# Kernel tuning notes

Hardware: AMD Instinct MI355X
Metric: run time of the kernel (lower is better)

## Reference

```python
import jax, jax.numpy as jnp
import numpy as np

# cost weights from __init__
W_CLASS = 1.0
W_KPTS = 1.0
W_CTRS = 1.0
W_DELTAS = 1.0
W_KPTS_CLASS = 1.0


def setup_inputs() -> dict:
    key = jax.random.key(0)
    k1, k2, k3, k4 = jax.random.split(key, 4)
    bs, Q, C, P = 16, 300, 2, 320
    pred_logits = jax.random.normal(k1, (bs, Q, C), dtype=jnp.float32)
    pred_kpts = jax.random.uniform(k2, (bs, Q, 53), dtype=jnp.float32)
    tgt_kpts = jax.random.uniform(k3, (P, 54), dtype=jnp.float32)
    # all visibility flags == 1 so the `if all(tgt_kpts[:,2])` branch is taken
    tgt_kpts = tgt_kpts.at[:, 2::3].set(1.0)
    tgt_ids = jax.random.randint(k4, (P,), 0, C)
    return {"pred_logits": pred_logits, "pred_kpts": pred_kpts,
            "tgt_kpts": tgt_kpts, "tgt_ids": tgt_ids}


def _cost_matrix(pred_logits, pred_kpts, tgt_kpts, tgt_ids):
    bs, Q, C = pred_logits.shape
    N = bs * Q
    P = tgt_kpts.shape[0]

    out_prob = jax.nn.softmax(pred_logits.reshape(N, C), axis=-1)  # [N,C]
    out_k = pred_kpts.reshape(N, -1)                               # [N,53]

    cost_class = -out_prob[:, tgt_ids]                             # [N,P]

    out_kpts_ids = out_k[:, 4::3]                                  # [N,17]
    tgt_kpts_ids = tgt_kpts[:, 5::3]                               # [P,17]

    x = jnp.concatenate([out_k[:, 0:1], out_k[:, 2::3]], axis=1)   # [N,18]
    y = jnp.concatenate([out_k[:, 1:2], out_k[:, 3::3]], axis=1)   # [N,18]
    x_abs = jnp.concatenate([x[:, 0:1], (x[:, 1:] - 0.5) * 2.0 + x[:, 0:1]], axis=1)
    y_abs = jnp.concatenate([y[:, 0:1], (y[:, 1:] - 0.5) * 2.0 + y[:, 0:1]], axis=1)

    tgt_x = tgt_kpts[:, 0::3]                                      # [P,18]
    tgt_y = tgt_kpts[:, 1::3]                                      # [P,18]
    tgt_x_abs = jnp.concatenate([tgt_x[:, 0:1], (tgt_x[:, 1:] - 0.5) * 2.0 + tgt_x[:, 0:1]], axis=1)
    tgt_y_abs = jnp.concatenate([tgt_y[:, 0:1], (tgt_y[:, 1:] - 0.5) * 2.0 + tgt_y[:, 0:1]], axis=1)

    vis = (tgt_kpts[:, 2::3] == 1.0).astype(pred_kpts.dtype)       # [P,18]
    visT = vis.T                                                   # [18,P]

    def interleave_pred(xc, yc):
        # [N,18,P] masked per target, interleaved to [N,36,P]
        mx = xc[:, :, None] * visT[None, :, :]
        my = yc[:, :, None] * visT[None, :, :]
        return jnp.stack([mx, my], axis=2).reshape(N, 36, P)

    def interleave_tgt(xc, yc):
        return jnp.stack([xc * vis, yc * vis], axis=2).reshape(P, 36)

    ok = interleave_pred(x, y)                 # [N,36,P]
    tk = interleave_tgt(tgt_x, tgt_y)          # [P,36]
    ok_abs = interleave_pred(x_abs, y_abs)     # [N,36,P]
    tk_abs = interleave_tgt(tgt_x_abs, tgt_y_abs)

    # vectorized version of the per-person cdist loop
    cost_deltas = jnp.abs(ok[:, 2:, :] - tk.T[None, 2:, :]).sum(axis=1)          # L1, [N,P]
    cost_kpts = jnp.abs(ok_abs[:, 2:, :] - tk_abs.T[None, 2:, :]).sum(axis=1)    # L1, [N,P]
    cost_ctrs = jnp.sqrt(((ok[:, :2, :] - tk.T[None, :2, :]) ** 2).sum(axis=1))  # L2, [N,P]
    cost_kpts_class = jnp.sqrt(((out_kpts_ids[:, None, :] - tgt_kpts_ids[None, :, :]) ** 2).sum(-1))  # [N,P]

    Cmat = (W_KPTS * cost_kpts + W_CTRS * cost_ctrs + W_DELTAS * cost_deltas
            + W_CLASS * cost_class + W_KPTS_CLASS * cost_kpts_class)
    return Cmat.reshape(bs, Q, P)


def reference(pred_logits, pred_kpts, tgt_kpts, tgt_ids):
    return _cost_matrix(pred_logits, pred_kpts, tgt_kpts, tgt_ids)
```

## Files before the change

kernel.cpp:

```cpp
#include <hip/hip_runtime.h>
#include <math.h>

#define BS 16
#define QN 300
#define CN 2
#define PN 320
#define NN (BS * QN)
#define KPRED 53
#define KTGT 54
#define TILE_N 4
#define STAGE_N (TILE_N * KPRED + TILE_N * CN)

__global__ __launch_bounds__(PN) void hungarian_cost_kernel(
    const float* __restrict__ pred_logits,
    const float* __restrict__ pred_kpts,
    const float* __restrict__ tgt_kpts,
    const int*   __restrict__ tgt_ids,
    float* __restrict__ out)
{
    __shared__ float sk[STAGE_N];
    const int p  = threadIdx.x;
    const int n0 = blockIdx.x * TILE_N;

    if (p < STAGE_N) {
        sk[p] = (p < TILE_N * KPRED)
                    ? pred_kpts[(size_t)n0 * KPRED + p]
                    : pred_logits[n0 * CN + (p - TILE_N * KPRED)];
    }

    float tx[18], ty[18], vjf[18], w[17];
    {
        const float* t = tgt_kpts + (size_t)p * KTGT;
        #pragma unroll
        for (int j = 0; j < 18; ++j) {
            tx[j] = t[3 * j];
            ty[j] = t[3 * j + 1];
            const float vv = t[3 * j + 2];
            vjf[j] = (vv == 1.0f) ? 1.0f : 0.0f;
            if (j >= 1) w[j - 1] = vv;
        }
    }
    const int cls = tgt_ids[p];

    __syncthreads();

    #pragma unroll
    for (int ni = 0; ni < TILE_N; ++ni) {
        const int n = n0 + ni;
        const float* k = &sk[ni * KPRED];

        const float dx0 = k[0] - tx[0];
        const float dy0 = k[1] - ty[0];

        float cd = 0.0f;
        float ck = 0.0f;
        float cq = 0.0f;
        #pragma unroll
        for (int j = 1; j < 18; ++j) {
            const float dx = k[3 * j - 1] - tx[j];
            const float dy = k[3 * j]     - ty[j];
            cd = fmaf(vjf[j], fabsf(dx) + fabsf(dy), cd);
            const float ax = fmaf(2.0f, dx, dx0);
            const float ay = fmaf(2.0f, dy, dy0);
            ck = fmaf(vjf[j], fabsf(ax) + fabsf(ay), ck);
            const float d = k[3 * j + 1] - w[j - 1];
            cq = fmaf(d, d, cq);
        }

        const float cc = vjf[0] * sqrtf(fmaf(dx0, dx0, dy0 * dy0));

        const float l0 = sk[TILE_N * KPRED + 2 * ni];
        const float l1 = sk[TILE_N * KPRED + 2 * ni + 1];
        const float m  = fmaxf(l0, l1);
        const float e0 = __expf(l0 - m);
        const float e1 = __expf(l1 - m);
        const float inv = 1.0f / (e0 + e1);
        const float ccls = -((cls == 0) ? e0 : e1) * inv;

        out[(size_t)n * PN + p] = ck + cc + cd + ccls + sqrtf(cq);
    }
}

extern "C" void kernel_launch(void* const* d_in, const int* in_sizes, int n_in,
                              void* d_out, int out_size, void* d_ws, size_t ws_size,
                              hipStream_t stream) {
    const float* pred_logits = (const float*)d_in[0];
    const float* pred_kpts   = (const float*)d_in[1];
    const float* tgt_kpts    = (const float*)d_in[2];
    const int*   tgt_ids     = (const int*)d_in[3];
    float* out = (float*)d_out;

    dim3 grid(NN / TILE_N);
    dim3 block(PN);
    hipLaunchKernelGGL(hungarian_cost_kernel, grid, block, 0, stream,
                       pred_logits, pred_kpts, tgt_kpts, tgt_ids, out);
}
```

Baseline: 75.06 us.

## Use persistent grid with double-buffered shared staging of prediction rows

Switches from one block per 4 prediction rows to a fixed grid of 960 blocks, each processing 5 rows strided by the grid size. The next row's keypoints and logits are prefetched into a second shared buffer while the current row is computed. The per-target registers are loaded once per block and reused across more rows, which cuts the redundant target loads the 1200-block launch performed. The cost is a block-wide barrier per row and fewer blocks in flight to hide memory latency.

```diff
diff --git a/kernel.cpp b/kernel.cpp
--- a/kernel.cpp
+++ b/kernel.cpp
@@ -8,8 +8,10 @@
 #define NN (BS * QN)
 #define KPRED 53
 #define KTGT 54
-#define TILE_N 4
-#define STAGE_N (TILE_N * KPRED + TILE_N * CN)
+
+#define GRID 960
+#define ROWS (NN / GRID)
+#define SROW 56
 
 __global__ __launch_bounds__(PN) void hungarian_cost_kernel(
     const float* __restrict__ pred_logits,
@@ -18,15 +20,9 @@
     const int*   __restrict__ tgt_ids,
     float* __restrict__ out)
 {
-    __shared__ float sk[STAGE_N];
-    const int p  = threadIdx.x;
-    const int n0 = blockIdx.x * TILE_N;
-
-    if (p < STAGE_N) {
-        sk[p] = (p < TILE_N * KPRED)
-                    ? pred_kpts[(size_t)n0 * KPRED + p]
-                    : pred_logits[n0 * CN + (p - TILE_N * KPRED)];
-    }
+    __shared__ float sk[2][SROW];
+    const int p   = threadIdx.x;
+    const int bid = blockIdx.x;
 
     float tx[18], ty[18], vjf[18], w[17];
     {
@@ -42,12 +38,22 @@
     }
     const int cls = tgt_ids[p];
 
+    if (p < KPRED)          sk[0][p] = pred_kpts[(size_t)bid * KPRED + p];
+    else if (p < KPRED + 2) sk[0][p] = pred_logits[(size_t)bid * CN + (p - KPRED)];
     __syncthreads();
 
     #pragma unroll
-    for (int ni = 0; ni < TILE_N; ++ni) {
-        const int n = n0 + ni;
-        const float* k = &sk[ni * KPRED];
+    for (int i = 0; i < ROWS; ++i) {
+        const int n   = bid + i * GRID;
+        const int cur = i & 1;
+
+        {
+            const int nn_ = (i + 1 < ROWS) ? (n + GRID) : n;
+            if (p < KPRED)          sk[cur ^ 1][p] = pred_kpts[(size_t)nn_ * KPRED + p];
+            else if (p < KPRED + 2) sk[cur ^ 1][p] = pred_logits[(size_t)nn_ * CN + (p - KPRED)];
+        }
+
+        const float* k = sk[cur];
 
         const float dx0 = k[0] - tx[0];
         const float dy0 = k[1] - ty[0];
@@ -69,15 +75,15 @@
 
         const float cc = vjf[0] * sqrtf(fmaf(dx0, dx0, dy0 * dy0));
 
-        const float l0 = sk[TILE_N * KPRED + 2 * ni];
-        const float l1 = sk[TILE_N * KPRED + 2 * ni + 1];
+        const float l0 = k[KPRED], l1 = k[KPRED + 1];
         const float m  = fmaxf(l0, l1);
         const float e0 = __expf(l0 - m);
         const float e1 = __expf(l1 - m);
-        const float inv = 1.0f / (e0 + e1);
-        const float ccls = -((cls == 0) ? e0 : e1) * inv;
+        const float ccls = -((cls == 0) ? e0 : e1) / (e0 + e1);
 
         out[(size_t)n * PN + p] = ck + cc + cd + ccls + sqrtf(cq);
+
+        __syncthreads();
     }
 }
 
@@ -90,8 +96,6 @@
     const int*   tgt_ids     = (const int*)d_in[3];
     float* out = (float*)d_out;
 
-    dim3 grid(NN / TILE_N);
-    dim3 block(PN);
-    hipLaunchKernelGGL(hungarian_cost_kernel, grid, block, 0, stream,
+    hipLaunchKernelGGL(hungarian_cost_kernel, dim3(GRID), dim3(PN), 0, stream,
                        pred_logits, pred_kpts, tgt_kpts, tgt_ids, out);
 }
```

Result: slower. 82.01 us (+9.3%).

## Drop LDS staging, read predictions directly and pack two rows into float2 math

Applied to the files above, without the earlier changes.

Removes the shared-memory staging of prediction keypoints and logits along with the block barrier. Each thread now reads the prediction values straight from global memory as uniform loads. The per-row arithmetic is paired across two query rows using 2-wide float vectors, so the compiler can emit packed FMA instructions. The cost is that every thread issues redundant global/scalar loads instead of LDS reads, and the gain depends on whether the compiler turns these into scalar loads and packed math.

```diff
diff --git a/kernel.cpp b/kernel.cpp
--- a/kernel.cpp
+++ b/kernel.cpp
@@ -9,7 +9,12 @@
 #define KPRED 53
 #define KTGT 54
 #define TILE_N 4
-#define STAGE_N (TILE_N * KPRED + TILE_N * CN)
+
+typedef float v2f __attribute__((ext_vector_type(2)));
+
+static __device__ __forceinline__ v2f fma2(v2f a, v2f b, v2f c) {
+    return __builtin_elementwise_fma(a, b, c);
+}
 
 __global__ __launch_bounds__(PN) void hungarian_cost_kernel(
     const float* __restrict__ pred_logits,
@@ -18,15 +23,8 @@
     const int*   __restrict__ tgt_ids,
     float* __restrict__ out)
 {
-    __shared__ float sk[STAGE_N];
     const int p  = threadIdx.x;
     const int n0 = blockIdx.x * TILE_N;
-
-    if (p < STAGE_N) {
-        sk[p] = (p < TILE_N * KPRED)
-                    ? pred_kpts[(size_t)n0 * KPRED + p]
-                    : pred_logits[n0 * CN + (p - TILE_N * KPRED)];
-    }
 
     float tx[18], ty[18], vjf[18], w[17];
     {
@@ -42,42 +40,64 @@
     }
     const int cls = tgt_ids[p];
 
-    __syncthreads();
+    #pragma unroll
+    for (int h = 0; h < TILE_N / 2; ++h) {
+        const int na = n0 + 2 * h;
+        const int nb = na + 1;
+        const float* ka = pred_kpts + (size_t)na * KPRED;
+        const float* kb = pred_kpts + (size_t)nb * KPRED;
 
-    #pragma unroll
-    for (int ni = 0; ni < TILE_N; ++ni) {
-        const int n = n0 + ni;
-        const float* k = &sk[ni * KPRED];
+        const v2f k0  = {ka[0], kb[0]};
+        const v2f k1  = {ka[1], kb[1]};
+        const v2f dx0 = k0 - (v2f){tx[0], tx[0]};
+        const v2f dy0 = k1 - (v2f){ty[0], ty[0]};
 
-        const float dx0 = k[0] - tx[0];
-        const float dy0 = k[1] - ty[0];
-
-        float cd = 0.0f;
-        float ck = 0.0f;
-        float cq = 0.0f;
+        v2f cd = {0.0f, 0.0f};
+        v2f ck = {0.0f, 0.0f};
+        v2f cq = {0.0f, 0.0f};
         #pragma unroll
         for (int j = 1; j < 18; ++j) {
-            const float dx = k[3 * j - 1] - tx[j];
-            const float dy = k[3 * j]     - ty[j];
-            cd = fmaf(vjf[j], fabsf(dx) + fabsf(dy), cd);
-            const float ax = fmaf(2.0f, dx, dx0);
-            const float ay = fmaf(2.0f, dy, dy0);
-            ck = fmaf(vjf[j], fabsf(ax) + fabsf(ay), ck);
-            const float d = k[3 * j + 1] - w[j - 1];
-            cq = fmaf(d, d, cq);
+            const v2f kx = {ka[3 * j - 1], kb[3 * j - 1]};
+            const v2f ky = {ka[3 * j],     kb[3 * j]};
+            const v2f kc = {ka[3 * j + 1], kb[3 * j + 1]};
+            const v2f vj2 = {vjf[j], vjf[j]};
+
+            const v2f dx = kx - (v2f){tx[j], tx[j]};
+            const v2f dy = ky - (v2f){ty[j], ty[j]};
+            const v2f adxy = {fabsf(dx.x) + fabsf(dy.x),
+                              fabsf(dx.y) + fabsf(dy.y)};
+            cd = fma2(vj2, adxy, cd);
+
+            const v2f ax = fma2((v2f){2.0f, 2.0f}, dx, dx0);
+            const v2f ay = fma2((v2f){2.0f, 2.0f}, dy, dy0);
+            const v2f aaxy = {fabsf(ax.x) + fabsf(ay.x),
+                              fabsf(ax.y) + fabsf(ay.y)};
+            ck = fma2(vj2, aaxy, ck);
+
+            const v2f d = kc - (v2f){w[j - 1], w[j - 1]};
+            cq = fma2(d, d, cq);
         }
 
-        const float cc = vjf[0] * sqrtf(fmaf(dx0, dx0, dy0 * dy0));
+        #pragma unroll
+        for (int r = 0; r < 2; ++r) {
+            const int n = (r == 0) ? na : nb;
+            const float dx0r = (r == 0) ? dx0.x : dx0.y;
+            const float dy0r = (r == 0) ? dy0.x : dy0.y;
+            const float cdr  = (r == 0) ? cd.x  : cd.y;
+            const float ckr  = (r == 0) ? ck.x  : ck.y;
+            const float cqr  = (r == 0) ? cq.x  : cq.y;
 
-        const float l0 = sk[TILE_N * KPRED + 2 * ni];
-        const float l1 = sk[TILE_N * KPRED + 2 * ni + 1];
-        const float m  = fmaxf(l0, l1);
-        const float e0 = __expf(l0 - m);
-        const float e1 = __expf(l1 - m);
-        const float inv = 1.0f / (e0 + e1);
-        const float ccls = -((cls == 0) ? e0 : e1) * inv;
+            const float cc = vjf[0] * sqrtf(fmaf(dx0r, dx0r, dy0r * dy0r));
 
-        out[(size_t)n * PN + p] = ck + cc + cd + ccls + sqrtf(cq);
+            const float l0 = pred_logits[n * CN + 0];
+            const float l1 = pred_logits[n * CN + 1];
+            const float m  = fmaxf(l0, l1);
+            const float e0 = __expf(l0 - m);
+            const float e1 = __expf(l1 - m);
+            const float ccls = -((cls == 0) ? e0 : e1) / (e0 + e1);
+
+            out[(size_t)n * PN + p] = ckr + cc + cdr + ccls + sqrtf(cqr);
+        }
     }
 }
 
@@ -90,8 +110,6 @@
     const int*   tgt_ids     = (const int*)d_in[3];
     float* out = (float*)d_out;
 
-    dim3 grid(NN / TILE_N);
-    dim3 block(PN);
-    hipLaunchKernelGGL(hungarian_cost_kernel, grid, block, 0, stream,
+    hipLaunchKernelGGL(hungarian_cost_kernel, dim3(NN / TILE_N), dim3(PN), 0, stream,
                        pred_logits, pred_kpts, tgt_kpts, tgt_ids, out);
 }
```

Measured after the change: 88.60 us. +18.0%, slower.
